# Kernel optimization log

Hardware: AMD Instinct MI355X
Metric: run time of the kernel (lower is better)

The kernel has to match this reference:

```python
import jax, jax.numpy as jnp
import numpy as np

NB_ATOMS = 128
NB_CH = 1
ATOM = 12          # atom_size
BATCH = 8
HW = 75            # -> 64x64 patch grid
LAM = 0.1          # soft-threshold level of the L1 proximal
UNROLL = 2         # unroll_steps
FISTA_ITERS = 15   # fixed inner FISTA iterations (replaces res-based stop)


def _prox(u):
    # soft-thresholding (prox of lam*||.||_1)
    return jnp.sign(u) * jnp.maximum(jnp.abs(u) - LAM, 0.0)


def _conv(x, w):
    # valid cross-correlation, NCHW / OIHW (== F.conv2d)
    return jax.lax.conv_general_dilated(x, w, (1, 1), 'VALID',
                                        dimension_numbers=('NCHW', 'OIHW', 'NCHW'))


def _fold(patches, H, W):
    # patches: [B, Ph, Pw, a, a] -> overlap-add to [B, 1, H, W] (== F.fold)
    B, Ph, Pw, a, _ = patches.shape
    out = jnp.zeros((B, H, W), patches.dtype)
    for di in range(a):              # fixed small kernel loop (a*a = 144 slots)
        for dj in range(a):
            out = out.at[:, di:di + Ph, dj:dj + Pw].add(patches[:, :, :, di, dj])
    return out[:, None]


def _fista(c0, X, q, mu):
    # standard FISTA on 0.5*||D^T c - y_patch||^2 + lam*||c||_1 with step mu
    def body(i, st):
        c, z, t = st
        cn = _prox(z - (z @ X - q) * mu)
        tn = (1.0 + jnp.sqrt(1.0 + 4.0 * t * t)) / 2.0
        zn = cn + ((t - 1.0) / tn) * (cn - c)
        return (cn, zn, tn)
    c, _, _ = jax.lax.fori_loop(0, FISTA_ITERS, body, (c0, c0, jnp.float32(1.0)))
    return c


def setup_inputs() -> dict:
    key = jax.random.key(0)
    k1, k2 = jax.random.split(key)
    y = jax.random.normal(k1, (BATCH, NB_CH, HW, HW), dtype=jnp.float32)
    atoms = jax.random.normal(k2, (NB_ATOMS, NB_CH, ATOM, ATOM), dtype=jnp.float32) / 1500.0
    beta = jnp.float32(0.1)
    mu = jnp.float32(1.0)
    return {"y": y, "atoms": atoms, "beta": beta, "mu": mu}


def reference(y, atoms, beta, mu):
    B, C, H, W = y.shape
    N, a = atoms.shape[0], atoms.shape[-1]
    beta = jax.nn.relu(beta)
    mu = jax.nn.relu(mu)
    # normalize atoms: zero-mean, unit L2 rows, then spectral norm / sqrt(mu)
    A = atoms - atoms.mean(axis=(1, 2, 3), keepdims=True)
    Af = A.reshape(N, -1)
    Af = Af / jnp.linalg.norm(Af, axis=1, keepdims=True)
    Af = Af / (jnp.linalg.norm(Af, ord=2) * jnp.sqrt(mu))
    atoms_n = Af.reshape(N, C, a, a)
    X = Af @ Af.T                                   # [N, N] gram
    Ph, Pw = H - a + 1, W - a + 1
    n_patch = B * Ph * Pw
    mean_filter = jnp.ones((1, 1, a, a), y.dtype) / (a * a)
    patch_mean = _conv(y, mean_filter).reshape(n_patch, 1, 1, 1)
    divisors = _fold(jnp.ones((B, Ph, Pw, a, a), y.dtype), H, W)  # overlap counts
    goal = y
    c = jnp.zeros((n_patch, N), y.dtype)
    sg = jax.lax.stop_gradient
    for _ in range(UNROLL):
        q = _conv(goal, atoms_n).transpose(0, 2, 3, 1).reshape(n_patch, N)
        cf = sg(_fista(sg(c), sg(X), sg(q), sg(mu)))   # torch.no_grad inner solve
        cf = _prox(cf - (cf @ X - q) * mu)             # one differentiable step
        pred = jnp.einsum('pn,ncij->pcij', cf, atoms_n) + patch_mean  # [P,1,a,a]
        pred = _fold(pred.reshape(B, Ph, Pw, a, a), H, W)
        goal = (y + beta * pred) / (1.0 + beta * divisors)
        c = cf
    return goal
```

## Files before the change

kernel.cpp:

```cpp
#include <hip/hip_runtime.h>
#include <stdint.h>

#define AA 144
#define LAM 0.1f

#define OFS_SC    0
#define OFS_AF1   64
#define OFS_G     36928
#define OFS_S0    53312
#define OFS_S1    69696
#define OFS_X     86080
#define OFS_PM    139328
#define OFS_GOAL  172096
#define OFS_CF    4411456
#define OFS_PRED  8605760
#define OFS_ATB   OFS_S0
#define OFS_ANTB  OFS_S1


typedef __attribute__((ext_vector_type(8))) short short8_t;
typedef __attribute__((ext_vector_type(4))) float f32x4;
typedef __attribute__((ext_vector_type(2))) float f32x2;

__device__ __forceinline__ unsigned short f2bf(float f) {
    union { float f; uint32_t u; } x; x.f = f;
    uint32_t u = x.u;
    return (unsigned short)((u + 0x7FFFu + ((u >> 16) & 1u)) >> 16);
}
__device__ __forceinline__ unsigned short f2bh(float f) {
    union { float f; uint32_t u; } x; x.f = f;
    return (unsigned short)((x.u + 0x8000u) >> 16);
}
__device__ __forceinline__ float bf2f(unsigned short u) {
    union { float f; uint32_t i; } x; x.i = ((uint32_t)u) << 16; return x.f;
}
__device__ __forceinline__ uint32_t pack_bf(float a, float b) {
    union { float f; uint32_t u; } xa, xb; xa.f = a; xb.f = b;
    return __builtin_amdgcn_perm(xb.u + 0x8000u, xa.u + 0x8000u, 0x07060302u);
}

#define PSTR 136
__global__ __launch_bounds__(1024) void k_setup(const float* atoms, const float* mu_p,
                                                float* ws, const float* y) {
    __shared__ unsigned short ABf[128 * 168];
    __shared__ unsigned short Pb[2][128 * PSTR];
    __shared__ float tr_arr[10];
    __shared__ float v[128];
    __shared__ float red[256];
    int t = threadIdx.x;
    if (blockIdx.x != 0) {
        int e = (blockIdx.x - 1) * 1024 + t;
        if (e < 45000) ws[OFS_GOAL + e] = y[e];
        if (e < 32768) {
            int b = e >> 12, pi = (e >> 6) & 63, pj = e & 63;
            const float* yb = y + b * 5625;
            float s = 0.f;
            for (int di = 0; di < 12; ++di) {
                const float* row = yb + (pi + di) * 75 + pj;
                #pragma unroll
                for (int dj = 0; dj < 12; ++dj) s += row[dj];
            }
            ws[OFS_PM + e] = s * (1.0f / 144.0f);
        }
        return;
    }
    int lane = t & 63, w = t >> 6;
    int col = lane & 15, quad = lane >> 4;
    if (t < 10) tr_arr[t] = (t == 0) ? 128.0f : 0.f;

    {
        int a = t >> 3, sub = t & 7;
        const float* ap = atoms + a * AA + sub * 18;
        float s = 0.f;
        #pragma unroll
        for (int k = 0; k < 18; ++k) s += ap[k];
        s += __shfl_xor(s, 1, 8); s += __shfl_xor(s, 2, 8); s += __shfl_xor(s, 4, 8);
        float mean = s * (1.0f / 144.0f);
        float ss = 0.f;
        #pragma unroll
        for (int k = 0; k < 18; ++k) { float d = ap[k] - mean; ss = fmaf(d, d, ss); }
        ss += __shfl_xor(ss, 1, 8); ss += __shfl_xor(ss, 2, 8); ss += __shfl_xor(ss, 4, 8);
        float rn = 1.0f / sqrtf(ss);
        #pragma unroll
        for (int k = 0; k < 18; ++k) {
            float av = (ap[k] - mean) * rn;
            ws[OFS_AF1 + a * AA + sub * 18 + k] = av;
            ABf[a * 168 + sub * 18 + k] = f2bf(av);
        }
        if (sub == 0) {
            #pragma unroll
            for (int k = AA; k < 160; ++k) ABf[a * 168 + k] = 0;
        }
    }
    __syncthreads();

    {
        uint32_t* D32 = (uint32_t*)Pb[0];
        float* G = ws + OFS_G;
        int mt = w & 7, gh = w >> 3;
        short8_t af[5];
        #pragma unroll
        for (int s = 0; s < 5; ++s)
            af[s] = *(const short8_t*)&ABf[(mt * 16 + col) * 168 + s * 32 + quad * 8];
        #pragma unroll
        for (int gi = 0; gi < 2; ++gi) {
            int g = gh * 2 + gi;
            short8_t b0[5], b1[5];
            #pragma unroll
            for (int s = 0; s < 5; ++s) {
                b0[s] = *(const short8_t*)&ABf[((2 * g) * 16 + col) * 168 + s * 32 + quad * 8];
                b1[s] = *(const short8_t*)&ABf[((2 * g + 1) * 16 + col) * 168 + s * 32 + quad * 8];
            }
            f32x4 a0 = (f32x4){0.f, 0.f, 0.f, 0.f};
            f32x4 a1 = (f32x4){0.f, 0.f, 0.f, 0.f};
            #pragma unroll
            for (int s = 0; s < 5; ++s) {
                a0 = __builtin_amdgcn_mfma_f32_16x16x32_bf16(af[s], b0[s], a0, 0, 0, 0);
                a1 = __builtin_amdgcn_mfma_f32_16x16x32_bf16(af[s], b1[s], a1, 0, 0, 0);
            }
            #pragma unroll
            for (int r = 0; r < 4; ++r) {
                int m = mt * 16 + quad * 4 + r;
                G[m * 128 + g * 32 + col] = a0[r];
                G[m * 128 + g * 32 + 16 + col] = a1[r];
                D32[m * 68 + g * 16 + col] = pack_bf(a0[r], a1[r]);
            }
        }
    }
    __syncthreads();

    int cur = 0;
    #pragma unroll 1
    for (int j = 0; j < 8; ++j) {
        float trn = tr_arr[j];
        float inv2 = 1.0f / (trn * trn);
        const unsigned short* S = Pb[cur];
        uint32_t* D32 = (uint32_t*)Pb[cur ^ 1];
        int mt = w & 7, nh = w >> 3;
        short8_t af[4];
        #pragma unroll
        for (int s = 0; s < 4; ++s)
            af[s] = *(const short8_t*)&S[(mt * 16 + col) * PSTR + s * 32 + quad * 8];
        #pragma unroll
        for (int pr = 0; pr < 2; ++pr) {
            int ntE = 4 * nh + 2 * pr, ntO = ntE + 1;
            short8_t bE[4], bO[4];
            #pragma unroll
            for (int s = 0; s < 4; ++s) {
                bE[s] = *(const short8_t*)&S[(ntE * 16 + col) * PSTR + s * 32 + quad * 8];
                bO[s] = *(const short8_t*)&S[(ntO * 16 + col) * PSTR + s * 32 + quad * 8];
            }
            f32x4 aE = (f32x4){0.f, 0.f, 0.f, 0.f};
            f32x4 aO = (f32x4){0.f, 0.f, 0.f, 0.f};
            #pragma unroll
            for (int s = 0; s < 4; ++s) {
                aE = __builtin_amdgcn_mfma_f32_16x16x32_bf16(af[s], bE[s], aE, 0, 0, 0);
                aO = __builtin_amdgcn_mfma_f32_16x16x32_bf16(af[s], bO[s], aO, 0, 0, 0);
            }
            int nE = ntE * 16 + col, nO = ntO * 16 + col;
            #pragma unroll
            for (int r = 0; r < 4; ++r) {
                float x0 = aE[r] * inv2, x1 = aO[r] * inv2;
                int row = mt * 16 + quad * 4 + r;
                D32[row * 68 + (ntE >> 1) * 16 + col] = pack_bf(x0, x1);
                if (row == nE) atomicAdd(&tr_arr[j + 1], x0);
                if (row == nO) atomicAdd(&tr_arr[j + 1], x1);
            }
        }
        __syncthreads();
        cur ^= 1;
    }

    {
        int a = t >> 3, sub = t & 7;
        const unsigned short* S = Pb[cur];
        float s = 0.f;
        #pragma unroll
        for (int k = 0; k < 16; ++k) s += bf2f(S[a * PSTR + sub * 16 + k]);
        s += __shfl_xor(s, 1, 8); s += __shfl_xor(s, 2, 8); s += __shfl_xor(s, 4, 8);
        if (sub == 0) v[a] = s;
    }
    __syncthreads();
    {
        int a = t >> 3, sub = t & 7;
        const float* G = ws + OFS_G;
        float wv = 0.f;
        #pragma unroll
        for (int k = 0; k < 16; ++k)
            wv = fmaf(G[a * 128 + sub * 16 + k], v[sub * 16 + k], wv);
        wv += __shfl_xor(wv, 1, 8); wv += __shfl_xor(wv, 2, 8); wv += __shfl_xor(wv, 4, 8);
        if (sub == 0) { red[a] = v[a] * wv; red[128 + a] = v[a] * v[a]; }
    }
    __syncthreads();
    for (int off = 64; off > 0; off >>= 1) {
        if (t < off) { red[t] += red[t + off]; red[128 + t] += red[128 + t + off]; }
        __syncthreads();
    }
    if (t == 0) {
        float lam = red[0] / red[128];
        float mu = fmaxf(mu_p[0], 0.0f);
        ws[OFS_SC + 16] = 1.0f / (lam * mu);
        ws[OFS_SC + 17] = 1.0f / (sqrtf(lam) * sqrtf(mu));
    }
}

__global__ __launch_bounds__(256) void k_finalize(float* ws) {
    int idx = blockIdx.x * 256 + threadIdx.x;
    float scX = ws[OFS_SC + 16], scA = ws[OFS_SC + 17];
    if (idx < 16384) {
        int n = idx >> 7, ks = idx & 127;
        int g = ks >> 5, rem = ks & 31, u = rem >> 1, v = rem & 1;
        int k = g * 32 + v * 16 + u;
        ((unsigned short*)(ws + OFS_X))[idx] = f2bf(ws[OFS_G + n * 128 + k] * scX);
    } else if (idx < 36864) {
        int e = idx - 16384;
        int n = e / 160, k = e - n * 160;
        float v = (k < 144) ? ws[OFS_AF1 + n * 144 + k] * scA : 0.f;
        ((unsigned short*)(ws + OFS_ATB))[e] = f2bf(v);
    } else {
        int e = idx - 36864;
        int jp = e >> 7, ks = e & 127;
        int g = ks >> 5, rem = ks & 31, u = rem >> 1, v = rem & 1;
        int n = g * 32 + v * 16 + u;
        ((unsigned short*)(ws + OFS_ANTB))[e] = f2bf(ws[OFS_AF1 + n * 144 + jp] * scA);
    }
}

__global__ __launch_bounds__(256) void k_fista(const unsigned short* XPB, const float* goal,
                                               const unsigned short* ATB,
                                               const unsigned short* ANTBP,
                                               const float* pm, uint32_t* cfgb,
                                               unsigned short* predh,
                                               const float* mu_p, int first, int write_cf) {
    __shared__ unsigned short Atile[32 * 168];
    __shared__ unsigned short Zbuf[2][32 * 136];
    int t = threadIdx.x;
    int lane = t & 63, w = t >> 6;
    int col = lane & 15, quad = lane >> 4;
    int nb = w * 32;
    int blk = blockIdx.x;
    int b = blk >> 7, pi = (blk >> 1) & 63, h = blk & 1;
    int p0 = blk * 32;
    float mu = fmaxf(mu_p[0], 0.0f);
    const f32x2 mu2 = (f32x2){mu, mu};
    const f32x2 lam2 = (f32x2){LAM, LAM};
    const f32x2 nlam2 = (f32x2){-LAM, -LAM};

    {
        const float* gb = goal + b * 5625 + pi * 75 + h * 32;
        uint32_t* A32 = (uint32_t*)Atile;
        #pragma unroll
        for (int i = 0; i < 10; ++i) {
            int pe = t + i * 256;
            int m = pe / 80, q32 = pe - m * 80;
            int kk = q32 * 2;
            float v0 = 0.f, v1 = 0.f;
            if (kk < 144) {
                int di = kk / 12, dj = kk - di * 12;
                v0 = gb[di * 75 + m + dj];
                int k1 = kk + 1, di1 = k1 / 12, dj1 = k1 - di1 * 12;
                v1 = gb[di1 * 75 + m + dj1];
            }
            A32[m * 84 + q32] = pack_bf(v0, v1);
        }
    }
    __syncthreads();

    f32x2 qv2[2][4];
    {
        short8_t bfq[2][5];
        #pragma unroll
        for (int nt = 0; nt < 2; ++nt)
            #pragma unroll
            for (int s = 0; s < 5; ++s)
                bfq[nt][s] = *(const short8_t*)&ATB[(nb + nt * 16 + col) * 160 + s * 32 + quad * 8];
        #pragma unroll
        for (int mt = 0; mt < 2; ++mt) {
            short8_t af[5];
            #pragma unroll
            for (int s = 0; s < 5; ++s)
                af[s] = *(const short8_t*)&Atile[(mt * 16 + col) * 168 + s * 32 + quad * 8];
            f32x4 acc0 = (f32x4){0.f, 0.f, 0.f, 0.f};
            f32x4 acc1 = (f32x4){0.f, 0.f, 0.f, 0.f};
            #pragma unroll
            for (int s = 0; s < 5; ++s) {
                acc0 = __builtin_amdgcn_mfma_f32_16x16x32_bf16(af[s], bfq[0][s], acc0, 0, 0, 0);
                acc1 = __builtin_amdgcn_mfma_f32_16x16x32_bf16(af[s], bfq[1][s], acc1, 0, 0, 0);
            }
            #pragma unroll
            for (int r = 0; r < 4; ++r) qv2[mt][r] = (f32x2){acc0[r], acc1[r]};
        }
    }

    short8_t xf[2][4];
    #pragma unroll
    for (int nt = 0; nt < 2; ++nt)
        #pragma unroll
        for (int s = 0; s < 4; ++s)
            xf[nt][s] = *(const short8_t*)&XPB[(nb + nt * 16 + col) * 128 + s * 32 + quad * 8];

    uint32_t* Z32w = (uint32_t*)Zbuf[0];
    f32x2 cv2[2][4], zo2[2][4];
    #pragma unroll
    for (int mt = 0; mt < 2; ++mt)
        #pragma unroll
        for (int r = 0; r < 4; ++r) {
            int row = mt * 16 + quad * 4 + r;
            uint32_t pk = 0u;
            float c0 = 0.f, c1 = 0.f;
            if (!first) {
                pk = cfgb[(p0 + row) * 64 + 16 * w + col];
                c0 = bf2f((unsigned short)(pk & 0xFFFFu));
                c1 = bf2f((unsigned short)(pk >> 16));
            }
            cv2[mt][r] = (f32x2){c0, c1};
            zo2[mt][r] = (f32x2){c0, c1};
            Z32w[row * 68 + 16 * w + col] = pk;
        }
    __syncthreads();

    f32x4 acc[2][2];
    auto matmul = [&](const unsigned short* Zr) {
        short8_t af[2][4];
        #pragma unroll
        for (int mt = 0; mt < 2; ++mt)
            #pragma unroll
            for (int s = 0; s < 4; ++s)
                af[mt][s] = *(const short8_t*)&Zr[(mt * 16 + col) * 136 + s * 32 + quad * 8];
        #pragma unroll
        for (int mt = 0; mt < 2; ++mt)
            #pragma unroll
            for (int nt = 0; nt < 2; ++nt)
                acc[mt][nt] = (f32x4){0.f, 0.f, 0.f, 0.f};
        #pragma unroll
        for (int s = 0; s < 4; ++s)
            #pragma unroll
            for (int mt = 0; mt < 2; ++mt)
                #pragma unroll
                for (int nt = 0; nt < 2; ++nt)
                    acc[mt][nt] = __builtin_amdgcn_mfma_f32_16x16x32_bf16(
                        af[mt][s], xf[nt][s], acc[mt][nt], 0, 0, 0);
    };

    float tm = 1.0f;
    int cur = 0;
    #pragma unroll 1
    for (int it = 0; it < 14; ++it) {
        matmul(Zbuf[cur]);
        float tnn = 0.5f * (1.0f + sqrtf(1.0f + 4.0f * tm * tm));
        float fm = (tm - 1.0f) / tnn;
        tm = tnn;
        f32x2 fm2 = (f32x2){fm, fm};
        uint32_t* Zw = (uint32_t*)Zbuf[cur ^ 1];
        #pragma unroll
        for (int mt = 0; mt < 2; ++mt)
            #pragma unroll
            for (int r = 0; r < 4; ++r) {
                f32x2 a2 = (f32x2){acc[mt][0][r], acc[mt][1][r]};
                f32x2 u2 = mu2 * (qv2[mt][r] - a2) + zo2[mt][r];
                f32x2 cl2 = __builtin_elementwise_min(
                                __builtin_elementwise_max(u2, nlam2), lam2);
                f32x2 cn2 = u2 - cl2;
                f32x2 zn2 = fm2 * (cn2 - cv2[mt][r]) + cn2;
                cv2[mt][r] = cn2;
                zo2[mt][r] = zn2;
                Zw[(mt * 16 + quad * 4 + r) * 68 + 16 * w + col] = pack_bf(zn2[0], zn2[1]);
            }
        __syncthreads();
        cur ^= 1;
    }
    {
        matmul(Zbuf[cur]);
        uint32_t* Zw = (uint32_t*)Zbuf[cur ^ 1];
        #pragma unroll
        for (int mt = 0; mt < 2; ++mt)
            #pragma unroll
            for (int r = 0; r < 4; ++r) {
                f32x2 a2 = (f32x2){acc[mt][0][r], acc[mt][1][r]};
                f32x2 u2 = mu2 * (qv2[mt][r] - a2) + zo2[mt][r];
                f32x2 cl2 = __builtin_elementwise_min(
                                __builtin_elementwise_max(u2, nlam2), lam2);
                f32x2 cn2 = u2 - cl2;
                cv2[mt][r] = cn2;
                Zw[(mt * 16 + quad * 4 + r) * 68 + 16 * w + col] = pack_bf(cn2[0], cn2[1]);
            }
        __syncthreads();
        cur ^= 1;
    }
    {
        matmul(Zbuf[cur]);
        uint32_t* Zw = (uint32_t*)Zbuf[cur ^ 1];
        #pragma unroll
        for (int mt = 0; mt < 2; ++mt)
            #pragma unroll
            for (int r = 0; r < 4; ++r) {
                int row = mt * 16 + quad * 4 + r;
                f32x2 a2 = (f32x2){acc[mt][0][r], acc[mt][1][r]};
                f32x2 u2 = mu2 * (qv2[mt][r] - a2) + cv2[mt][r];
                f32x2 cl2 = __builtin_elementwise_min(
                                __builtin_elementwise_max(u2, nlam2), lam2);
                f32x2 cf2 = u2 - cl2;
                uint32_t pk = pack_bf(cf2[0], cf2[1]);
                if (write_cf) cfgb[(p0 + row) * 64 + 16 * w + col] = pk;
                Zw[row * 68 + 16 * w + col] = pk;
            }
        __syncthreads();
        cur ^= 1;
    }

    {
        int jt0 = (w == 0) ? 0 : (2 * w + 1);
        int jtn = (w == 0) ? 3 : 2;
        const unsigned short* Zr = Zbuf[cur];
        short8_t af[2][4];
        #pragma unroll
        for (int mt = 0; mt < 2; ++mt)
            #pragma unroll
            for (int s = 0; s < 4; ++s)
                af[mt][s] = *(const short8_t*)&Zr[(mt * 16 + col) * 136 + s * 32 + quad * 8];
        f32x4 accp[2][3];
        #pragma unroll
        for (int mt = 0; mt < 2; ++mt)
            #pragma unroll
            for (int ji = 0; ji < 3; ++ji)
                accp[mt][ji] = (f32x4){0.f, 0.f, 0.f, 0.f};
        #pragma unroll
        for (int ji = 0; ji < 3; ++ji) {
            if (ji < jtn) {
                int jt = jt0 + ji;
                short8_t bf4[4];
                #pragma unroll
                for (int s = 0; s < 4; ++s)
                    bf4[s] = *(const short8_t*)&ANTBP[(jt * 16 + col) * 128 + s * 32 + quad * 8];
                #pragma unroll
                for (int mt = 0; mt < 2; ++mt)
                    #pragma unroll
                    for (int s = 0; s < 4; ++s)
                        accp[mt][ji] = __builtin_amdgcn_mfma_f32_16x16x32_bf16(
                            af[mt][s], bf4[s], accp[mt][ji], 0, 0, 0);
            }
        }
        #pragma unroll
        for (int mt = 0; mt < 2; ++mt)
            #pragma unroll
            for (int r = 0; r < 4; ++r) {
                int p = p0 + mt * 16 + quad * 4 + r;
                float pmv = pm[p];
                #pragma unroll
                for (int ji = 0; ji < 3; ++ji)
                    if (ji < jtn)
                        predh[p * 144 + (jt0 + ji) * 16 + col] = f2bh(accp[mt][ji][r] + pmv);
            }
    }
}

__global__ __launch_bounds__(256) void k_fold(const float* y, const float* beta_p,
                                              const unsigned short* predh, float* goal,
                                              float* out, int write_out) {
    __shared__ float P[12 * 832];
    int i = blockIdx.x, b = blockIdx.y;
    int t = threadIdx.x;
    for (int di = 0; di < 12; ++di) {
        int pi = i - di;
        if ((unsigned)pi >= 64u) continue;
        int base = (b << 12) + (pi << 6);
        #pragma unroll
        for (int it = 0; it < 3; ++it) {
            int e = t + it * 256;
            int pj = e / 12, dj = e - pj * 12;
            P[di * 832 + pj * 13 + dj] = bf2f(predh[(base + pj) * AA + di * 12 + dj]);
        }
    }
    __syncthreads();
    if (t >= 75) return;
    int j = t;
    float S = 0.f;
    for (int di = 0; di < 12; ++di) {
        if ((unsigned)(i - di) >= 64u) continue;
        const float* Pd = &P[di * 832];
        #pragma unroll
        for (int dj = 0; dj < 12; ++dj) {
            int pj = j - dj;
            if ((unsigned)pj >= 64u) continue;
            S += Pd[pj * 13 + dj];
        }
    }
    int ci = min(i, 11) - max(i - 63, 0) + 1;
    int cj = min(j, 11) - max(j - 63, 0) + 1;
    float beta = fmaxf(beta_p[0], 0.0f);
    int idx = i * 75 + j;
    float yv = y[b * 5625 + idx];
    float g = (yv + beta * S) / (1.0f + beta * (float)(ci * cj));
    if (write_out) out[b * 5625 + idx] = g;
    else           goal[b * 5625 + idx] = g;
}

extern "C" void kernel_launch(void* const* d_in, const int* in_sizes, int n_in,
                              void* d_out, int out_size, void* d_ws, size_t ws_size,
                              hipStream_t stream) {
    const float* y     = (const float*)d_in[0];
    const float* atoms = (const float*)d_in[1];
    const float* beta  = (const float*)d_in[2];
    const float* mu    = (const float*)d_in[3];
    float* out = (float*)d_out;
    float* ws = (float*)d_ws;

    k_setup<<<46, 1024, 0, stream>>>(atoms, mu, ws, y);
    k_finalize<<<216, 256, 0, stream>>>(ws);

    for (int u = 0; u < 2; ++u) {
        k_fista<<<1024, 256, 0, stream>>>((const unsigned short*)(ws + OFS_X),
                                          ws + OFS_GOAL,
                                          (const unsigned short*)(ws + OFS_ATB),
                                          (const unsigned short*)(ws + OFS_ANTB),
                                          ws + OFS_PM, (uint32_t*)(ws + OFS_CF),
                                          (unsigned short*)(ws + OFS_PRED),
                                          mu, u == 0 ? 1 : 0, u == 0 ? 1 : 0);
        k_fold<<<dim3(75, 8), 256, 0, stream>>>(y, beta,
                                                (const unsigned short*)(ws + OFS_PRED),
                                                ws + OFS_GOAL, out, u == 1 ? 1 : 0);
    }
}
```

Before: 213.7 us.

## Restructure FISTA as single-wave transposed MFMA with register-resident iterates

The FISTA kernel is rewritten so each 64-thread wave owns 16 patches and all 128 atoms. It computes the transposed product X·Zᵀ so the MFMA output layout matches the next B-operand, which keeps the iterate in registers and removes the LDS round trips and block barriers. The mu and negative scaling are folded into the precomputed X and q matrices, so q seeds the accumulator directly. Packing uses the hardware bf16 convert instruction, and predictions are stored in a slot-major layout for coalesced access in fold. The cost is higher register pressure, since X fragments and all 128 coefficients per lane are held in registers.

```diff
diff --git a/kernel.cpp b/kernel.cpp
--- a/kernel.cpp
+++ b/kernel.cpp
@@ -21,6 +21,7 @@
 typedef __attribute__((ext_vector_type(8))) short short8_t;
 typedef __attribute__((ext_vector_type(4))) float f32x4;
 typedef __attribute__((ext_vector_type(2))) float f32x2;
+typedef __attribute__((ext_vector_type(4))) uint32_t u32x4;
 
 __device__ __forceinline__ unsigned short f2bf(float f) {
     union { float f; uint32_t u; } x; x.f = f;
@@ -37,6 +38,11 @@
 __device__ __forceinline__ uint32_t pack_bf(float a, float b) {
     union { float f; uint32_t u; } xa, xb; xa.f = a; xb.f = b;
     return __builtin_amdgcn_perm(xb.u + 0x8000u, xa.u + 0x8000u, 0x07060302u);
+}
+__device__ __forceinline__ uint32_t cvt_pk(float a, float b) {
+    uint32_t r;
+    asm("v_cvt_pk_bf16_f32 %0, %1, %2" : "=v"(r) : "v"(a), "v"(b));
+    return r;
 }
 
 #define PSTR 136
@@ -199,258 +205,197 @@
     if (t == 0) {
         float lam = red[0] / red[128];
         float mu = fmaxf(mu_p[0], 0.0f);
-        ws[OFS_SC + 16] = 1.0f / (lam * mu);
-        ws[OFS_SC + 17] = 1.0f / (sqrtf(lam) * sqrtf(mu));
+        float scX = 1.0f / (lam * mu);
+        float scA = 1.0f / (sqrtf(lam) * sqrtf(mu));
+        ws[OFS_SC + 16] = scX * mu;
+        ws[OFS_SC + 17] = scA;
+        ws[OFS_SC + 18] = -scA * mu;
     }
 }
 
 __global__ __launch_bounds__(256) void k_finalize(float* ws) {
     int idx = blockIdx.x * 256 + threadIdx.x;
-    float scX = ws[OFS_SC + 16], scA = ws[OFS_SC + 17];
+    float scX = ws[OFS_SC + 16], scA = ws[OFS_SC + 17], scQ = ws[OFS_SC + 18];
     if (idx < 16384) {
-        int n = idx >> 7, ks = idx & 127;
-        int g = ks >> 5, rem = ks & 31, u = rem >> 1, v = rem & 1;
-        int k = g * 32 + v * 16 + u;
-        ((unsigned short*)(ws + OFS_X))[idx] = f2bf(ws[OFS_G + n * 128 + k] * scX);
+        int row = idx >> 7, ks = idx & 127;
+        int s = ks >> 5, Q = (ks >> 3) & 3, j = ks & 7;
+        int n = 32 * s + 16 * (j >> 2) + 4 * Q + (j & 3);
+        ((unsigned short*)(ws + OFS_X))[idx] = f2bf(ws[OFS_G + row * 128 + n] * scX);
     } else if (idx < 36864) {
         int e = idx - 16384;
         int n = e / 160, k = e - n * 160;
-        float v = (k < 144) ? ws[OFS_AF1 + n * 144 + k] * scA : 0.f;
+        float v = (k < 144) ? ws[OFS_AF1 + n * 144 + k] * scQ : 0.f;
         ((unsigned short*)(ws + OFS_ATB))[e] = f2bf(v);
     } else {
         int e = idx - 36864;
-        int jp = e >> 7, ks = e & 127;
-        int g = ks >> 5, rem = ks & 31, u = rem >> 1, v = rem & 1;
-        int n = g * 32 + v * 16 + u;
-        ((unsigned short*)(ws + OFS_ANTB))[e] = f2bf(ws[OFS_AF1 + n * 144 + jp] * scA);
-    }
-}
-
-__global__ __launch_bounds__(256) void k_fista(const unsigned short* XPB, const float* goal,
-                                               const unsigned short* ATB,
-                                               const unsigned short* ANTBP,
-                                               const float* pm, uint32_t* cfgb,
-                                               unsigned short* predh,
-                                               const float* mu_p, int first, int write_cf) {
-    __shared__ unsigned short Atile[32 * 168];
-    __shared__ unsigned short Zbuf[2][32 * 136];
-    int t = threadIdx.x;
-    int lane = t & 63, w = t >> 6;
-    int col = lane & 15, quad = lane >> 4;
-    int nb = w * 32;
-    int blk = blockIdx.x;
-    int b = blk >> 7, pi = (blk >> 1) & 63, h = blk & 1;
-    int p0 = blk * 32;
-    float mu = fmaxf(mu_p[0], 0.0f);
-    const f32x2 mu2 = (f32x2){mu, mu};
-    const f32x2 lam2 = (f32x2){LAM, LAM};
-    const f32x2 nlam2 = (f32x2){-LAM, -LAM};
-
-    {
-        const float* gb = goal + b * 5625 + pi * 75 + h * 32;
-        uint32_t* A32 = (uint32_t*)Atile;
-        #pragma unroll
-        for (int i = 0; i < 10; ++i) {
-            int pe = t + i * 256;
-            int m = pe / 80, q32 = pe - m * 80;
-            int kk = q32 * 2;
+        int jr = e >> 7, ks = e & 127;
+        int s = ks >> 5, Q = (ks >> 3) & 3, j = ks & 7;
+        int n = 32 * s + 16 * (j >> 2) + 4 * Q + (j & 3);
+        ((unsigned short*)(ws + OFS_ANTB))[e] = f2bf(ws[OFS_AF1 + n * 144 + jr] * scA);
+    }
+}
+
+__global__ __launch_bounds__(64, 1) void k_fista(const unsigned short* XPB,
+        const float* goal, const unsigned short* ATB, const unsigned short* ANTBP,
+        const float* pm, uint32_t* cfgb, unsigned short* predh,
+        int first, int write_cf) {
+    int lane = threadIdx.x & 63;
+    int col = lane & 15, Q = lane >> 4;
+    int wid = blockIdx.x;
+    int b = wid >> 8, pi = (wid >> 2) & 63;
+    int pcol = (wid & 3) * 16 + col;
+    int p = wid * 16 + col;
+    const float* gb = goal + b * 5625 + pi * 75;
+
+    u32x4 bq[5];
+    #pragma unroll
+    for (int s = 0; s < 5; ++s)
+        #pragma unroll
+        for (int jj = 0; jj < 4; ++jj) {
+            int k0 = 32 * s + 8 * Q + 2 * jj;
             float v0 = 0.f, v1 = 0.f;
-            if (kk < 144) {
-                int di = kk / 12, dj = kk - di * 12;
-                v0 = gb[di * 75 + m + dj];
-                int k1 = kk + 1, di1 = k1 / 12, dj1 = k1 - di1 * 12;
-                v1 = gb[di1 * 75 + m + dj1];
-            }
-            A32[m * 84 + q32] = pack_bf(v0, v1);
-        }
-    }
-    __syncthreads();
-
-    f32x2 qv2[2][4];
-    {
-        short8_t bfq[2][5];
-        #pragma unroll
-        for (int nt = 0; nt < 2; ++nt)
-            #pragma unroll
-            for (int s = 0; s < 5; ++s)
-                bfq[nt][s] = *(const short8_t*)&ATB[(nb + nt * 16 + col) * 160 + s * 32 + quad * 8];
-        #pragma unroll
-        for (int mt = 0; mt < 2; ++mt) {
-            short8_t af[5];
-            #pragma unroll
-            for (int s = 0; s < 5; ++s)
-                af[s] = *(const short8_t*)&Atile[(mt * 16 + col) * 168 + s * 32 + quad * 8];
-            f32x4 acc0 = (f32x4){0.f, 0.f, 0.f, 0.f};
-            f32x4 acc1 = (f32x4){0.f, 0.f, 0.f, 0.f};
-            #pragma unroll
-            for (int s = 0; s < 5; ++s) {
-                acc0 = __builtin_amdgcn_mfma_f32_16x16x32_bf16(af[s], bfq[0][s], acc0, 0, 0, 0);
-                acc1 = __builtin_amdgcn_mfma_f32_16x16x32_bf16(af[s], bfq[1][s], acc1, 0, 0, 0);
-            }
-            #pragma unroll
-            for (int r = 0; r < 4; ++r) qv2[mt][r] = (f32x2){acc0[r], acc1[r]};
-        }
-    }
-
-    short8_t xf[2][4];
+            if (k0 < 144) {
+                int di = k0 / 12, dj = k0 - di * 12;
+                const float* r = gb + di * 75 + pcol + dj;
+                v0 = r[0]; v1 = r[1];
+            }
+            bq[s][jj] = cvt_pk(v0, v1);
+        }
+
+    f32x4 qn4[8];
     #pragma unroll
-    for (int nt = 0; nt < 2; ++nt)
+    for (int m = 0; m < 8; ++m) {
+        short8_t af[5];
+        #pragma unroll
+        for (int s = 0; s < 5; ++s)
+            af[s] = *(const short8_t*)&ATB[(m * 16 + col) * 160 + 32 * s + 8 * Q];
+        f32x4 a = (f32x4){0.f, 0.f, 0.f, 0.f};
+        #pragma unroll
+        for (int s = 0; s < 5; ++s)
+            a = __builtin_amdgcn_mfma_f32_16x16x32_bf16(af[s],
+                    __builtin_bit_cast(short8_t, bq[s]), a, 0, 0, 0);
+        qn4[m] = a;
+    }
+
+    short8_t xf[8][4];
+    #pragma unroll
+    for (int m = 0; m < 8; ++m)
         #pragma unroll
         for (int s = 0; s < 4; ++s)
-            xf[nt][s] = *(const short8_t*)&XPB[(nb + nt * 16 + col) * 128 + s * 32 + quad * 8];
-
-    uint32_t* Z32w = (uint32_t*)Zbuf[0];
-    f32x2 cv2[2][4], zo2[2][4];
-    #pragma unroll
-    for (int mt = 0; mt < 2; ++mt)
-        #pragma unroll
-        for (int r = 0; r < 4; ++r) {
-            int row = mt * 16 + quad * 4 + r;
-            uint32_t pk = 0u;
-            float c0 = 0.f, c1 = 0.f;
-            if (!first) {
-                pk = cfgb[(p0 + row) * 64 + 16 * w + col];
-                c0 = bf2f((unsigned short)(pk & 0xFFFFu));
-                c1 = bf2f((unsigned short)(pk >> 16));
-            }
-            cv2[mt][r] = (f32x2){c0, c1};
-            zo2[mt][r] = (f32x2){c0, c1};
-            Z32w[row * 68 + 16 * w + col] = pk;
-        }
-    __syncthreads();
-
-    f32x4 acc[2][2];
-    auto matmul = [&](const unsigned short* Zr) {
-        short8_t af[2][4];
-        #pragma unroll
-        for (int mt = 0; mt < 2; ++mt)
+            xf[m][s] = *(const short8_t*)&XPB[(m * 16 + col) * 128 + 32 * s + 8 * Q];
+
+    f32x4 c4[8], z4[8], acc4[8];
+    u32x4 bfr[4];
+    if (first) {
+        #pragma unroll
+        for (int m = 0; m < 8; ++m) c4[m] = z4[m] = (f32x4){0.f, 0.f, 0.f, 0.f};
+        #pragma unroll
+        for (int s = 0; s < 4; ++s) bfr[s] = (u32x4){0u, 0u, 0u, 0u};
+    } else {
+        const u32x4* cp = (const u32x4*)(cfgb + ((size_t)wid * 64 + lane) * 16);
+        #pragma unroll
+        for (int s = 0; s < 4; ++s) {
+            u32x4 v = cp[s];
+            bfr[s] = v;
+            #pragma unroll
+            for (int jj = 0; jj < 4; ++jj) {
+                int m = (s << 1) | (jj >> 1), r = 2 * (jj & 1);
+                uint32_t pk = v[jj];
+                c4[m][r]     = __builtin_bit_cast(float, pk << 16);
+                c4[m][r + 1] = __builtin_bit_cast(float, pk & 0xFFFF0000u);
+            }
+        }
+        #pragma unroll
+        for (int m = 0; m < 8; ++m) z4[m] = c4[m];
+    }
+
+    const f32x4 lamP = (f32x4){LAM, LAM, LAM, LAM};
+    const f32x4 lamN = (f32x4){-LAM, -LAM, -LAM, -LAM};
+
+    auto matmul = [&]() {
+        #pragma unroll
+        for (int m = 0; m < 8; ++m)
+            acc4[m] = __builtin_amdgcn_mfma_f32_16x16x32_bf16(xf[m][0],
+                          __builtin_bit_cast(short8_t, bfr[0]), qn4[m], 0, 0, 0);
+        #pragma unroll
+        for (int s = 1; s < 4; ++s)
+            #pragma unroll
+            for (int m = 0; m < 8; ++m)
+                acc4[m] = __builtin_amdgcn_mfma_f32_16x16x32_bf16(xf[m][s],
+                              __builtin_bit_cast(short8_t, bfr[s]), acc4[m], 0, 0, 0);
+    };
+    auto pack = [&](f32x4 (&src)[8]) {
+        #pragma unroll
+        for (int s = 0; s < 4; ++s)
+            #pragma unroll
+            for (int jj = 0; jj < 4; ++jj) {
+                int m = (s << 1) | (jj >> 1), r = 2 * (jj & 1);
+                bfr[s][jj] = cvt_pk(src[m][r], src[m][r + 1]);
+            }
+    };
+
+    float tm = 1.0f;
+    #pragma unroll 2
+    for (int it = 0; it < 14; ++it) {
+        matmul();
+        float tn = 0.5f * (1.0f + sqrtf(1.0f + 4.0f * tm * tm));
+        float fm = (tm - 1.0f) / tn;
+        tm = tn;
+        f32x4 fm4 = (f32x4){fm, fm, fm, fm};
+        #pragma unroll
+        for (int m = 0; m < 8; ++m) {
+            f32x4 u = z4[m] - acc4[m];
+            f32x4 cl = __builtin_elementwise_min(__builtin_elementwise_max(u, lamN), lamP);
+            f32x4 cn = u - cl;
+            z4[m] = cn + fm4 * (cn - c4[m]);
+            c4[m] = cn;
+        }
+        pack(z4);
+    }
+    {
+        matmul();
+        #pragma unroll
+        for (int m = 0; m < 8; ++m) {
+            f32x4 u = z4[m] - acc4[m];
+            f32x4 cl = __builtin_elementwise_min(__builtin_elementwise_max(u, lamN), lamP);
+            c4[m] = u - cl;
+        }
+        pack(c4);
+    }
+    {
+        matmul();
+        #pragma unroll
+        for (int m = 0; m < 8; ++m) {
+            f32x4 u = c4[m] - acc4[m];
+            f32x4 cl = __builtin_elementwise_min(__builtin_elementwise_max(u, lamN), lamP);
+            c4[m] = u - cl;
+        }
+        pack(c4);
+    }
+    if (write_cf) {
+        u32x4* cp = (u32x4*)(cfgb + ((size_t)wid * 64 + lane) * 16);
+        #pragma unroll
+        for (int s = 0; s < 4; ++s) cp[s] = bfr[s];
+    }
+
+    {
+        float pmv = pm[p];
+        f32x4 pm4 = (f32x4){pmv, pmv, pmv, pmv};
+        #pragma unroll
+        for (int jm = 0; jm < 9; ++jm) {
+            short8_t anf[4];
             #pragma unroll
             for (int s = 0; s < 4; ++s)
-                af[mt][s] = *(const short8_t*)&Zr[(mt * 16 + col) * 136 + s * 32 + quad * 8];
-        #pragma unroll
-        for (int mt = 0; mt < 2; ++mt)
-            #pragma unroll
-            for (int nt = 0; nt < 2; ++nt)
-                acc[mt][nt] = (f32x4){0.f, 0.f, 0.f, 0.f};
-        #pragma unroll
-        for (int s = 0; s < 4; ++s)
-            #pragma unroll
-            for (int mt = 0; mt < 2; ++mt)
-                #pragma unroll
-                for (int nt = 0; nt < 2; ++nt)
-                    acc[mt][nt] = __builtin_amdgcn_mfma_f32_16x16x32_bf16(
-                        af[mt][s], xf[nt][s], acc[mt][nt], 0, 0, 0);
-    };
-
-    float tm = 1.0f;
-    int cur = 0;
-    #pragma unroll 1
-    for (int it = 0; it < 14; ++it) {
-        matmul(Zbuf[cur]);
-        float tnn = 0.5f * (1.0f + sqrtf(1.0f + 4.0f * tm * tm));
-        float fm = (tm - 1.0f) / tnn;
-        tm = tnn;
-        f32x2 fm2 = (f32x2){fm, fm};
-        uint32_t* Zw = (uint32_t*)Zbuf[cur ^ 1];
-        #pragma unroll
-        for (int mt = 0; mt < 2; ++mt)
-            #pragma unroll
-            for (int r = 0; r < 4; ++r) {
-                f32x2 a2 = (f32x2){acc[mt][0][r], acc[mt][1][r]};
-                f32x2 u2 = mu2 * (qv2[mt][r] - a2) + zo2[mt][r];
-                f32x2 cl2 = __builtin_elementwise_min(
-                                __builtin_elementwise_max(u2, nlam2), lam2);
-                f32x2 cn2 = u2 - cl2;
-                f32x2 zn2 = fm2 * (cn2 - cv2[mt][r]) + cn2;
-                cv2[mt][r] = cn2;
-                zo2[mt][r] = zn2;
-                Zw[(mt * 16 + quad * 4 + r) * 68 + 16 * w + col] = pack_bf(zn2[0], zn2[1]);
-            }
-        __syncthreads();
-        cur ^= 1;
-    }
-    {
-        matmul(Zbuf[cur]);
-        uint32_t* Zw = (uint32_t*)Zbuf[cur ^ 1];
-        #pragma unroll
-        for (int mt = 0; mt < 2; ++mt)
-            #pragma unroll
-            for (int r = 0; r < 4; ++r) {
-                f32x2 a2 = (f32x2){acc[mt][0][r], acc[mt][1][r]};
-                f32x2 u2 = mu2 * (qv2[mt][r] - a2) + zo2[mt][r];
-                f32x2 cl2 = __builtin_elementwise_min(
-                                __builtin_elementwise_max(u2, nlam2), lam2);
-                f32x2 cn2 = u2 - cl2;
-                cv2[mt][r] = cn2;
-                Zw[(mt * 16 + quad * 4 + r) * 68 + 16 * w + col] = pack_bf(cn2[0], cn2[1]);
-            }
-        __syncthreads();
-        cur ^= 1;
-    }
-    {
-        matmul(Zbuf[cur]);
-        uint32_t* Zw = (uint32_t*)Zbuf[cur ^ 1];
-        #pragma unroll
-        for (int mt = 0; mt < 2; ++mt)
-            #pragma unroll
-            for (int r = 0; r < 4; ++r) {
-                int row = mt * 16 + quad * 4 + r;
-                f32x2 a2 = (f32x2){acc[mt][0][r], acc[mt][1][r]};
-                f32x2 u2 = mu2 * (qv2[mt][r] - a2) + cv2[mt][r];
-                f32x2 cl2 = __builtin_elementwise_min(
-                                __builtin_elementwise_max(u2, nlam2), lam2);
-                f32x2 cf2 = u2 - cl2;
-                uint32_t pk = pack_bf(cf2[0], cf2[1]);
-                if (write_cf) cfgb[(p0 + row) * 64 + 16 * w + col] = pk;
-                Zw[row * 68 + 16 * w + col] = pk;
-            }
-        __syncthreads();
-        cur ^= 1;
-    }
-
-    {
-        int jt0 = (w == 0) ? 0 : (2 * w + 1);
-        int jtn = (w == 0) ? 3 : 2;
-        const unsigned short* Zr = Zbuf[cur];
-        short8_t af[2][4];
-        #pragma unroll
-        for (int mt = 0; mt < 2; ++mt)
+                anf[s] = *(const short8_t*)&ANTBP[(jm * 16 + col) * 128 + 32 * s + 8 * Q];
+            f32x4 a = pm4;
             #pragma unroll
             for (int s = 0; s < 4; ++s)
-                af[mt][s] = *(const short8_t*)&Zr[(mt * 16 + col) * 136 + s * 32 + quad * 8];
-        f32x4 accp[2][3];
-        #pragma unroll
-        for (int mt = 0; mt < 2; ++mt)
-            #pragma unroll
-            for (int ji = 0; ji < 3; ++ji)
-                accp[mt][ji] = (f32x4){0.f, 0.f, 0.f, 0.f};
-        #pragma unroll
-        for (int ji = 0; ji < 3; ++ji) {
-            if (ji < jtn) {
-                int jt = jt0 + ji;
-                short8_t bf4[4];
-                #pragma unroll
-                for (int s = 0; s < 4; ++s)
-                    bf4[s] = *(const short8_t*)&ANTBP[(jt * 16 + col) * 128 + s * 32 + quad * 8];
-                #pragma unroll
-                for (int mt = 0; mt < 2; ++mt)
-                    #pragma unroll
-                    for (int s = 0; s < 4; ++s)
-                        accp[mt][ji] = __builtin_amdgcn_mfma_f32_16x16x32_bf16(
-                            af[mt][s], bf4[s], accp[mt][ji], 0, 0, 0);
-            }
-        }
-        #pragma unroll
-        for (int mt = 0; mt < 2; ++mt)
-            #pragma unroll
-            for (int r = 0; r < 4; ++r) {
-                int p = p0 + mt * 16 + quad * 4 + r;
-                float pmv = pm[p];
-                #pragma unroll
-                for (int ji = 0; ji < 3; ++ji)
-                    if (ji < jtn)
-                        predh[p * 144 + (jt0 + ji) * 16 + col] = f2bh(accp[mt][ji][r] + pmv);
-            }
+                a = __builtin_amdgcn_mfma_f32_16x16x32_bf16(anf[s],
+                        __builtin_bit_cast(short8_t, bfr[s]), a, 0, 0, 0);
+            #pragma unroll
+            for (int r = 0; r < 4; ++r)
+                predh[(jm * 16 + 4 * Q + r) * 32768 + p] = f2bh(a[r]);
+        }
     }
 }
 
@@ -467,8 +412,8 @@
         #pragma unroll
         for (int it = 0; it < 3; ++it) {
             int e = t + it * 256;
-            int pj = e / 12, dj = e - pj * 12;
-            P[di * 832 + pj * 13 + dj] = bf2f(predh[(base + pj) * AA + di * 12 + dj]);
+            int dj = e >> 6, pj = e & 63;
+            P[di * 832 + pj * 13 + dj] = bf2f(predh[(di * 12 + dj) * 32768 + base + pj]);
         }
     }
     __syncthreads();
@@ -509,13 +454,13 @@
     k_finalize<<<216, 256, 0, stream>>>(ws);
 
     for (int u = 0; u < 2; ++u) {
-        k_fista<<<1024, 256, 0, stream>>>((const unsigned short*)(ws + OFS_X),
-                                          ws + OFS_GOAL,
-                                          (const unsigned short*)(ws + OFS_ATB),
-                                          (const unsigned short*)(ws + OFS_ANTB),
-                                          ws + OFS_PM, (uint32_t*)(ws + OFS_CF),
-                                          (unsigned short*)(ws + OFS_PRED),
-                                          mu, u == 0 ? 1 : 0, u == 0 ? 1 : 0);
+        k_fista<<<2048, 64, 0, stream>>>((const unsigned short*)(ws + OFS_X),
+                                         ws + OFS_GOAL,
+                                         (const unsigned short*)(ws + OFS_ATB),
+                                         (const unsigned short*)(ws + OFS_ANTB),
+                                         ws + OFS_PM, (uint32_t*)(ws + OFS_CF),
+                                         (unsigned short*)(ws + OFS_PRED),
+                                         u == 0 ? 1 : 0, u == 0 ? 1 : 0);
         k_fold<<<dim3(75, 8), 256, 0, stream>>>(y, beta,
                                                 (const unsigned short*)(ws + OFS_PRED),
                                                 ws + OFS_GOAL, out, u == 1 ? 1 : 0);
```

After: 204.1 us. 4.5% less time.
